# Kernel tuning notes

Measured on AMD Instinct MI355X. Metric: run time of the kernel, lower is better.

Reference implementation:

```python
import jax, jax.numpy as jnp
import numpy as np

N_NODES = 50000
N_EDGES = 800000
IN_DIM = 128
EMB = 128
EDGE_DIM = 16
N_LAYERS = 4
BATCH = 64


def setup_inputs() -> dict:
    key = jax.random.key(0)
    ks = jax.random.split(key, 12)
    x = jax.random.normal(ks[0], (N_NODES, IN_DIM), dtype=jnp.float32)
    edge_index = jax.random.randint(ks[1], (2, N_EDGES), 0, N_NODES, dtype=jnp.int64)
    edge_attr = jax.random.normal(ks[2], (N_EDGES, EDGE_DIM), dtype=jnp.float32)
    batch = jnp.sort(jax.random.randint(ks[3], (N_NODES,), 0, BATCH, dtype=jnp.int64))

    def glorot(k, shape):
        fan_in = shape[-2]
        return jax.random.normal(k, shape, dtype=jnp.float32) / jnp.sqrt(jnp.float32(fan_in))

    msg_in = 2 * EMB + EDGE_DIM  # [h_src, h_dst, edge_attr]
    upd_in = 2 * EMB             # [h, aggregated_messages]
    return {
        "x": x,
        "edge_index": edge_index,
        "edge_attr": edge_attr,
        "batch": batch,
        "W_in": glorot(ks[4], (IN_DIM, EMB)),
        "b_in": jnp.zeros((EMB,), jnp.float32),
        "W_msg": glorot(ks[5], (N_LAYERS, msg_in, EMB)),
        "b_msg": jnp.zeros((N_LAYERS, EMB), jnp.float32),
        "W_upd": glorot(ks[6], (N_LAYERS, upd_in, EMB)),
        "b_upd": jnp.zeros((N_LAYERS, EMB), jnp.float32),
        "W_pred": glorot(ks[7], (EMB, 1)),
        "b_pred": jnp.zeros((1,), jnp.float32),
    }


def reference(x, edge_index, edge_attr, batch,
              W_in, b_in, W_msg, b_msg, W_upd, b_upd, W_pred, b_pred):
    n_nodes = x.shape[0]
    src, dst = edge_index[0], edge_index[1]

    # lin_in
    h = x @ W_in + b_in  # [N, EMB]

    # stacked message-passing layers with residual adds
    for l in range(W_msg.shape[0]):  # small fixed layer loop
        # per-edge message: relu(Linear([h_src, h_dst, e]))
        m_in = jnp.concatenate([h[src], h[dst], edge_attr], axis=-1)  # [E, 2*EMB+ED]
        m = jax.nn.relu(m_in @ W_msg[l] + b_msg[l])                    # [E, EMB]
        # sum-aggregate messages at destination nodes
        agg = jax.ops.segment_sum(m, dst, num_segments=n_nodes)       # [N, EMB]
        # node update: relu(Linear([h, agg])); residual add (h = h + conv(h))
        u_in = jnp.concatenate([h, agg], axis=-1)                      # [N, 2*EMB]
        h = h + jax.nn.relu(u_in @ W_upd[l] + b_upd[l])

    # global mean pool over graphs in the batch
    counts = jax.ops.segment_sum(jnp.ones((n_nodes,), h.dtype), batch, num_segments=BATCH)
    h_graph = jax.ops.segment_sum(h, batch, num_segments=BATCH) / jnp.maximum(counts, 1.0)[:, None]

    # lin_pred + view(-1)
    out = h_graph @ W_pred + b_pred  # [BATCH, 1]
    return out.reshape(-1)
```

## Files before the change

### kernel.cpp

```cpp
#include <hip/hip_runtime.h>


#define THREADS 256

typedef __attribute__((ext_vector_type(8))) short short8v;
typedef __attribute__((ext_vector_type(4))) float f32x4;

__device__ inline unsigned short f2bf(float f)
{
    unsigned int u = __float_as_uint(f);
    return (unsigned short)((u + 0x7FFFu + ((u >> 16) & 1u)) >> 16);
}

__global__ __launch_bounds__(THREADS)
void wconv_all(const float* __restrict__ W_in, const float* __restrict__ W_msg,
               const float* __restrict__ W_upd, unsigned short* __restrict__ wbf)
{
    int b = blockIdx.x;
    int job, kb;
    if (b < 576) { job = b >> 6; kb = b & 63; }
    else         { int r = b - 576; job = 9 + (r >> 7); kb = r & 127; }

    const float* src;
    unsigned short* dst;
    int K;
    if (job == 0)      { src = W_in;                                  dst = wbf;                       K = 128; }
    else if (job <= 4) { int l = job - 1; src = W_msg + (size_t)l * 272 * 128;             dst = wbf + 16384  + l * 16384; K = 128; }
    else if (job <= 8) { int l = job - 5; src = W_msg + (size_t)l * 272 * 128 + 128 * 128; dst = wbf + 81920  + l * 16384; K = 128; }
    else               { int l = job - 9; src = W_upd + (size_t)l * 256 * 128;             dst = wbf + 147456 + l * 32768; K = 256; }

    int i = kb * 256 + threadIdx.x;
    int k = i >> 7, n = i & 127;
    dst[n * K + k] = f2bf(src[i]);
}

__global__ __launch_bounds__(THREADS)
void f32_to_bf16(const float* __restrict__ in, unsigned short* __restrict__ out, int n4)
{
    int i = blockIdx.x * blockDim.x + threadIdx.x;
    int stride = gridDim.x * blockDim.x;
    for (; i < n4; i += stride) {
        float4 v = reinterpret_cast<const float4*>(in)[i];
        unsigned int lo = f2bf(v.x) | ((unsigned int)f2bf(v.y) << 16);
        unsigned int hi = f2bf(v.z) | ((unsigned int)f2bf(v.w) << 16);
        reinterpret_cast<uint2*>(out)[i] = make_uint2(lo, hi);
    }
}

template<bool RELU, bool RESID, bool WF32>
__global__ __launch_bounds__(THREADS)
void gemm_bf16(const unsigned short* __restrict__ X1, const unsigned short* __restrict__ X2,
               const unsigned short* __restrict__ Wt, const float* __restrict__ bias,
               const float* __restrict__ resid, float* __restrict__ Cf,
               unsigned short* __restrict__ Cbf, int M, int K)
{
    __shared__ unsigned short Als[64 * 40];
    __shared__ unsigned short Bls[128 * 40];

    const int t = threadIdx.x;
    const int w = t >> 6;
    const int l = t & 63;
    const int r  = l & 15;
    const int kb = l >> 4;
    const int mBase = blockIdx.x * 64;

    f32x4 acc[8];
#pragma unroll
    for (int c = 0; c < 8; c++) acc[c] = (f32x4){0.f, 0.f, 0.f, 0.f};

    const int am = t >> 2;
    const int ak = (t & 3) * 8;
    const int agr = min(mBase + am, M - 1);

    const int c0 = t, c1 = t + 256;
    const int bn0 = c0 >> 2, bk0 = (c0 & 3) * 8;
    const int bn1 = c1 >> 2, bk1 = (c1 & 3) * 8;

    for (int k0 = 0; k0 < K; k0 += 32) {
        const unsigned short* Xs = X1;
        int ko = k0;
        if (k0 >= 128) { Xs = X2; ko = k0 - 128; }

        short8v xv  = *reinterpret_cast<const short8v*>(Xs + (size_t)agr * 128 + ko + ak);
        short8v wv0 = *reinterpret_cast<const short8v*>(Wt + (size_t)bn0 * K + k0 + bk0);
        short8v wv1 = *reinterpret_cast<const short8v*>(Wt + (size_t)bn1 * K + k0 + bk1);

        __syncthreads();

        *reinterpret_cast<short8v*>(&Als[am * 40 + ak])   = xv;
        *reinterpret_cast<short8v*>(&Bls[bn0 * 40 + bk0]) = wv0;
        *reinterpret_cast<short8v*>(&Bls[bn1 * 40 + bk1]) = wv1;

        __syncthreads();

        const short8v a = *reinterpret_cast<const short8v*>(&Als[(w * 16 + r) * 40 + kb * 8]);
#pragma unroll
        for (int c = 0; c < 8; c++) {
            const short8v b = *reinterpret_cast<const short8v*>(&Bls[(c * 16 + r) * 40 + kb * 8]);
            acc[c] = __builtin_amdgcn_mfma_f32_16x16x32_bf16(a, b, acc[c], 0, 0, 0);
        }
    }

    const int rbase = mBase + w * 16 + kb * 4;
#pragma unroll
    for (int c = 0; c < 8; c++) {
        const int gc = c * 16 + r;
        float bv = bias ? bias[gc] : 0.f;
#pragma unroll
        for (int j = 0; j < 4; j++) {
            int gr = rbase + j;
            if (gr >= M) continue;
            float v = acc[c][j] + bv;
            if (RELU)  v = fmaxf(v, 0.f);
            if (RESID) v += resid[(size_t)gr * 128 + gc];
            if (WF32)  Cf[(size_t)gr * 128 + gc] = v;
            Cbf[(size_t)gr * 128 + gc] = f2bf(v);
        }
    }
}

__global__ __launch_bounds__(THREADS)
void zero_i32(int* __restrict__ p, int n)
{
    int i = blockIdx.x * blockDim.x + threadIdx.x;
    int stride = gridDim.x * blockDim.x;
    for (; i < n; i += stride) p[i] = 0;
}


__global__ __launch_bounds__(THREADS)
void csr_hist(const int* __restrict__ edst, int* __restrict__ deg, int nE)
{
    int i = blockIdx.x * blockDim.x + threadIdx.x;
    int stride = gridDim.x * blockDim.x;
    for (; i < nE; i += stride) atomicAdd(&deg[edst[i]], 1);
}

__global__ __launch_bounds__(THREADS)
void scan_stage1(const int* __restrict__ deg, int* __restrict__ incl,
                 int* __restrict__ psum, int n)
{
    __shared__ int buf[THREADS];
    const int t = threadIdx.x;
    const int base = blockIdx.x * 1024 + t * 4;

    int v0 = (base + 0 < n) ? deg[base + 0] : 0;
    int v1 = (base + 1 < n) ? deg[base + 1] : 0;
    int v2 = (base + 2 < n) ? deg[base + 2] : 0;
    int v3 = (base + 3 < n) ? deg[base + 3] : 0;
    const int s = v0 + v1 + v2 + v3;

    buf[t] = s;
    __syncthreads();
#pragma unroll
    for (int off = 1; off < THREADS; off <<= 1) {
        int x = (t >= off) ? buf[t - off] : 0;
        __syncthreads();
        buf[t] += x;
        __syncthreads();
    }
    const int excl = buf[t] - s;

    if (base + 0 < n) incl[base + 0] = excl + v0;
    if (base + 1 < n) incl[base + 1] = excl + v0 + v1;
    if (base + 2 < n) incl[base + 2] = excl + v0 + v1 + v2;
    if (base + 3 < n) incl[base + 3] = excl + s;
    if (t == THREADS - 1) psum[blockIdx.x] = buf[THREADS - 1];
}

__global__ __launch_bounds__(THREADS)
void scan_stage2(int* __restrict__ psum, int nb)
{
    __shared__ int buf[THREADS];
    const int t = threadIdx.x;
    int v = (t < nb) ? psum[t] : 0;
    buf[t] = v;
    __syncthreads();
#pragma unroll
    for (int off = 1; off < THREADS; off <<= 1) {
        int x = (t >= off) ? buf[t - off] : 0;
        __syncthreads();
        buf[t] += x;
        __syncthreads();
    }
    if (t < nb) psum[t] = buf[t] - v;
}

__global__ __launch_bounds__(THREADS)
void scan_stage3(const int* __restrict__ incl, const int* __restrict__ deg,
                 const int* __restrict__ psum, int* __restrict__ rowptr,
                 int* __restrict__ wp, int n, int nE)
{
    int i = blockIdx.x * blockDim.x + threadIdx.x;
    int stride = gridDim.x * blockDim.x;
    for (; i < n; i += stride) {
        int ex = incl[i] - deg[i] + psum[i >> 10];
        rowptr[i] = ex;
        wp[i]     = ex;
    }
    if (blockIdx.x == 0 && threadIdx.x == 0) rowptr[n] = nE;
}

__global__ __launch_bounds__(THREADS)
void csr_scatter(const int* __restrict__ esrc, const int* __restrict__ edst,
                 const float* __restrict__ eattr, int* __restrict__ wp,
                 int* __restrict__ col, float* __restrict__ eattrp, int nE)
{
    int i = blockIdx.x * blockDim.x + threadIdx.x;
    int stride = gridDim.x * blockDim.x;
    for (; i < nE; i += stride) {
        int d = edst[i];
        int pos = atomicAdd(&wp[d], 1);
        col[pos] = esrc[i];
        const float4* src4 = reinterpret_cast<const float4*>(eattr + (size_t)i * 16);
        float4*       dst4 = reinterpret_cast<float4*>(eattrp + (size_t)pos * 16);
        dst4[0] = src4[0]; dst4[1] = src4[1]; dst4[2] = src4[2]; dst4[3] = src4[3];
    }
}

__global__ __launch_bounds__(THREADS)
void edge_agg(const unsigned short* __restrict__ A, const unsigned short* __restrict__ Bb,
              const float* __restrict__ eattrp, const int* __restrict__ col,
              const int* __restrict__ rowptr, const float* __restrict__ Wm3,
              unsigned short* __restrict__ agg, int nN)
{
    __shared__ float W3s[16 * 128];
    const int t = threadIdx.x;

    *reinterpret_cast<float4*>(&W3s[t * 4])        = *reinterpret_cast<const float4*>(Wm3 + t * 4);
    *reinterpret_cast<float4*>(&W3s[1024 + t * 4]) = *reinterpret_cast<const float4*>(Wm3 + 1024 + t * 4);
    __syncthreads();

    const int lane = t & 63;
    const int wid  = __builtin_amdgcn_readfirstlane(t >> 6);
    const int d    = blockIdx.x * 4 + wid;
    if (d >= nN) return;

    float2 w[16];
#pragma unroll
    for (int k = 0; k < 16; k++)
        w[k] = *reinterpret_cast<const float2*>(&W3s[k * 128 + lane * 2]);

    const unsigned int bu = *reinterpret_cast<const unsigned int*>(Bb + (size_t)d * 128 + lane * 2);
    const float b0 = __uint_as_float(bu << 16);
    const float b1 = __uint_as_float(bu & 0xFFFF0000u);
    float2 acc = make_float2(0.f, 0.f);

    const int beg = rowptr[d], end = rowptr[d + 1];
    for (int e = beg; e < end; e++) {
        const int s = col[e];
        const unsigned int au = *reinterpret_cast<const unsigned int*>(A + (size_t)s * 128 + lane * 2);
        float vx = __uint_as_float(au << 16) + b0;
        float vy = __uint_as_float(au & 0xFFFF0000u) + b1;
        const float4* ea4 = reinterpret_cast<const float4*>(eattrp + (size_t)e * 16);
        const float4 e0 = ea4[0], e1 = ea4[1], e2 = ea4[2], e3 = ea4[3];
        const float ek[16] = {e0.x, e0.y, e0.z, e0.w, e1.x, e1.y, e1.z, e1.w,
                              e2.x, e2.y, e2.z, e2.w, e3.x, e3.y, e3.z, e3.w};
#pragma unroll
        for (int k = 0; k < 16; k++) {
            vx = fmaf(ek[k], w[k].x, vx);
            vy = fmaf(ek[k], w[k].y, vy);
        }
        acc.x += fmaxf(vx, 0.f);
        acc.y += fmaxf(vy, 0.f);
    }
    unsigned int o = (unsigned int)f2bf(acc.x) | ((unsigned int)f2bf(acc.y) << 16);
    *reinterpret_cast<unsigned int*>(agg + (size_t)d * 128 + lane * 2) = o;
}


__global__ __launch_bounds__(THREADS)
void pool_partial(const float* __restrict__ h, const int* __restrict__ batch,
                  float* __restrict__ hgsum, int n)
{
    const int t    = threadIdx.x;
    const int c    = t & 127;
    const int half = t >> 7;
    const int beg  = blockIdx.x * 256;
    const int end  = min(beg + 256, n);
    if (beg >= n) return;

    int   cur = -1;
    float acc = 0.f;
    for (int r = beg + half; r < end; r += 2) {
        int g = batch[r];
        if (g != cur) {
            if (cur >= 0) atomicAdd(&hgsum[(size_t)cur * 128 + c], acc);
            cur = g; acc = 0.f;
        }
        acc += h[(size_t)r * 128 + c];
    }
    if (cur >= 0) atomicAdd(&hgsum[(size_t)cur * 128 + c], acc);
}

__global__ __launch_bounds__(THREADS)
void pool_final(const float* __restrict__ hgsum, const int* __restrict__ batch,
                const float* __restrict__ Wp, const float* __restrict__ bp,
                float* __restrict__ out, int n)
{
    __shared__ float red[128];
    const int g = blockIdx.x;
    const int t = threadIdx.x;
    if (t >= 128) return;

    int lo, hi;
    {
        int a = 0, b = n;
        while (a < b) { int m = (a + b) >> 1; if (batch[m] < g) a = m + 1; else b = m; }
        lo = a;
        b = n;
        while (a < b) { int m = (a + b) >> 1; if (batch[m] < g + 1) a = m + 1; else b = m; }
        hi = a;
    }
    const int cnt = hi - lo;

    float v = hgsum[(size_t)g * 128 + t] / (float)max(cnt, 1);
    red[t] = v * Wp[t];
    __syncthreads();
    for (int off = 64; off > 0; off >>= 1) {
        if (t < off) red[t] += red[t + off];
        __syncthreads();
    }
    if (t == 0) out[g] = red[0] + bp[0];
}

extern "C" void kernel_launch(void* const* d_in, const int* in_sizes, int n_in,
                              void* d_out, int out_size, void* d_ws, size_t ws_size,
                              hipStream_t stream)
{
    const float* x      = (const float*)d_in[0];
    const int*   ei     = (const int*)  d_in[1];
    const float* eattr  = (const float*)d_in[2];
    const int*   batch  = (const int*)  d_in[3];
    const float* W_in   = (const float*)d_in[4];
    const float* b_in   = (const float*)d_in[5];
    const float* W_msg  = (const float*)d_in[6];
    const float* b_msg  = (const float*)d_in[7];
    const float* W_upd  = (const float*)d_in[8];
    const float* b_upd  = (const float*)d_in[9];
    const float* W_pred = (const float*)d_in[10];
    const float* b_pred = (const float*)d_in[11];
    float* out = (float*)d_out;

    const int nN = in_sizes[0] / 128;
    const int nE = in_sizes[1] / 2;
    const int* esrc = ei;
    const int* edst = ei + nE;

    float* h      = (float*)d_ws;
    float* eattrp = h + (size_t)nN * 128;
    float* hgsum  = eattrp + (size_t)nE * 16;
    unsigned short* xbf    = (unsigned short*)(hgsum + 8192);
    unsigned short* h_bf   = xbf    + (size_t)nN * 128;
    unsigned short* A_bf   = h_bf   + (size_t)nN * 128;
    unsigned short* Bb_bf  = A_bf   + (size_t)nN * 128;
    unsigned short* agg_bf = Bb_bf  + (size_t)nN * 128;
    unsigned short* wbf    = agg_bf + (size_t)nN * 128;
    unsigned short* wt_in  = wbf;
    unsigned short* wt_m1  = wbf + 16384;
    unsigned short* wt_m2  = wbf + 81920;
    unsigned short* wt_up  = wbf + 147456;
    int*   rowptr = (int*)(wbf + 278528);
    int*   wp     = rowptr + (nN + 1);
    int*   deg    = wp     + nN;
    int*   incl   = deg    + nN;
    int*   psum   = incl   + nN;
    int*   col    = psum   + 256;

    dim3 blk(THREADS);
    const int gx = (nN + 63) / 64;
    const int nChunks = (nN + 1023) / 1024;

    wconv_all<<<1088, blk, 0, stream>>>(W_in, W_msg, W_upd, wbf);
    f32_to_bf16<<<1024, blk, 0, stream>>>(x, xbf, nN * 128 / 4);

    zero_i32<<<64, blk, 0, stream>>>(deg, nN);
    csr_hist<<<256, blk, 0, stream>>>(edst, deg, nE);
    scan_stage1<<<nChunks, blk, 0, stream>>>(deg, incl, psum, nN);
    scan_stage2<<<1, blk, 0, stream>>>(psum, nChunks);
    scan_stage3<<<64, blk, 0, stream>>>(incl, deg, psum, rowptr, wp, nN, nE);
    csr_scatter<<<256, blk, 0, stream>>>(esrc, edst, eattr, wp, col, eattrp, nE);

    gemm_bf16<false, false, true><<<gx, blk, 0, stream>>>(xbf, nullptr, wt_in, b_in, nullptr, h, h_bf, nN, 128);

    for (int l = 0; l < 4; l++) {
        const float* Wm3 = W_msg + (size_t)l * 272 * 128 + 256 * 128;
        const float* bm  = b_msg + l * 128;
        const float* bu  = b_upd + l * 128;

        gemm_bf16<false, false, false><<<gx, blk, 0, stream>>>(h_bf, nullptr, wt_m1 + l * 16384, nullptr, nullptr, nullptr, A_bf,  nN, 128);
        gemm_bf16<false, false, false><<<gx, blk, 0, stream>>>(h_bf, nullptr, wt_m2 + l * 16384, bm,      nullptr, nullptr, Bb_bf, nN, 128);

        edge_agg<<<(nN + 3) / 4, blk, 0, stream>>>(A_bf, Bb_bf, eattrp, col, rowptr, Wm3, agg_bf, nN);

        gemm_bf16<true, true, true><<<gx, blk, 0, stream>>>(h_bf, agg_bf, wt_up + l * 32768, bu, h, h, h_bf, nN, 256);
    }

    zero_i32<<<16, blk, 0, stream>>>((int*)hgsum, 64 * 128);
    pool_partial<<<(nN + 255) / 256, blk, 0, stream>>>(h, batch, hgsum, nN);
    pool_final<<<64, blk, 0, stream>>>(hgsum, batch, W_pred, b_pred, out, nN);
}
```

Baseline: 666.7 us.

## Load GEMM operands directly into registers and unroll edge aggregation by two

The bf16 GEMM drops its LDS staging and both __syncthreads. Each wave now loads its A rows and the weight fragments straight from global memory into MFMA operand registers. Each wave computes 32 rows with two accumulator sets, so the block tile grows to 128 rows, and K becomes a template parameter. The edge aggregation loop also processes two edges per iteration to expose more memory-level parallelism, at the cost of more register pressure and redundant weight reads from L1/L2 across waves.

```diff
diff --git a/kernel.cpp b/kernel.cpp
--- a/kernel.cpp
+++ b/kernel.cpp
@@ -47,74 +47,63 @@
     }
 }
 
-template<bool RELU, bool RESID, bool WF32>
-__global__ __launch_bounds__(THREADS)
-void gemm_bf16(const unsigned short* __restrict__ X1, const unsigned short* __restrict__ X2,
-               const unsigned short* __restrict__ Wt, const float* __restrict__ bias,
-               const float* __restrict__ resid, float* __restrict__ Cf,
-               unsigned short* __restrict__ Cbf, int M, int K)
-{
-    __shared__ unsigned short Als[64 * 40];
-    __shared__ unsigned short Bls[128 * 40];
-
+template<bool RELU, bool RESID, bool WF32, int K>
+__global__ __launch_bounds__(THREADS, 2)
+void gemm_direct(const unsigned short* __restrict__ X1, const unsigned short* __restrict__ X2,
+                 const unsigned short* __restrict__ Wt, const float* __restrict__ bias,
+                 const float* __restrict__ resid, float* __restrict__ Cf,
+                 unsigned short* __restrict__ Cbf, int M)
+{
     const int t = threadIdx.x;
     const int w = t >> 6;
     const int l = t & 63;
     const int r  = l & 15;
     const int kb = l >> 4;
-    const int mBase = blockIdx.x * 64;
-
-    f32x4 acc[8];
-#pragma unroll
-    for (int c = 0; c < 8; c++) acc[c] = (f32x4){0.f, 0.f, 0.f, 0.f};
-
-    const int am = t >> 2;
-    const int ak = (t & 3) * 8;
-    const int agr = min(mBase + am, M - 1);
-
-    const int c0 = t, c1 = t + 256;
-    const int bn0 = c0 >> 2, bk0 = (c0 & 3) * 8;
-    const int bn1 = c1 >> 2, bk1 = (c1 & 3) * 8;
+    const int mBase = blockIdx.x * 128 + w * 32;
+
+    f32x4 acc[2][8];
+#pragma unroll
+    for (int mi = 0; mi < 2; mi++)
+#pragma unroll
+        for (int c = 0; c < 8; c++) acc[mi][c] = (f32x4){0.f, 0.f, 0.f, 0.f};
+
+    const int row0 = min(mBase + r,      M - 1);
+    const int row1 = min(mBase + 16 + r, M - 1);
 
     for (int k0 = 0; k0 < K; k0 += 32) {
         const unsigned short* Xs = X1;
         int ko = k0;
-        if (k0 >= 128) { Xs = X2; ko = k0 - 128; }
-
-        short8v xv  = *reinterpret_cast<const short8v*>(Xs + (size_t)agr * 128 + ko + ak);
-        short8v wv0 = *reinterpret_cast<const short8v*>(Wt + (size_t)bn0 * K + k0 + bk0);
-        short8v wv1 = *reinterpret_cast<const short8v*>(Wt + (size_t)bn1 * K + k0 + bk1);
-
-        __syncthreads();
-
-        *reinterpret_cast<short8v*>(&Als[am * 40 + ak])   = xv;
-        *reinterpret_cast<short8v*>(&Bls[bn0 * 40 + bk0]) = wv0;
-        *reinterpret_cast<short8v*>(&Bls[bn1 * 40 + bk1]) = wv1;
-
-        __syncthreads();
-
-        const short8v a = *reinterpret_cast<const short8v*>(&Als[(w * 16 + r) * 40 + kb * 8]);
+        if (K == 256 && k0 >= 128) { Xs = X2; ko = k0 - 128; }
+        const int kk = ko + kb * 8;
+
+        const short8v a0 = *reinterpret_cast<const short8v*>(Xs + (size_t)row0 * 128 + kk);
+        const short8v a1 = *reinterpret_cast<const short8v*>(Xs + (size_t)row1 * 128 + kk);
+
 #pragma unroll
         for (int c = 0; c < 8; c++) {
-            const short8v b = *reinterpret_cast<const short8v*>(&Bls[(c * 16 + r) * 40 + kb * 8]);
-            acc[c] = __builtin_amdgcn_mfma_f32_16x16x32_bf16(a, b, acc[c], 0, 0, 0);
+            const short8v b = *reinterpret_cast<const short8v*>(Wt + (size_t)(c * 16 + r) * K + k0 + kb * 8);
+            acc[0][c] = __builtin_amdgcn_mfma_f32_16x16x32_bf16(a0, b, acc[0][c], 0, 0, 0);
+            acc[1][c] = __builtin_amdgcn_mfma_f32_16x16x32_bf16(a1, b, acc[1][c], 0, 0, 0);
         }
     }
 
-    const int rbase = mBase + w * 16 + kb * 4;
-#pragma unroll
-    for (int c = 0; c < 8; c++) {
-        const int gc = c * 16 + r;
-        float bv = bias ? bias[gc] : 0.f;
-#pragma unroll
-        for (int j = 0; j < 4; j++) {
-            int gr = rbase + j;
-            if (gr >= M) continue;
-            float v = acc[c][j] + bv;
-            if (RELU)  v = fmaxf(v, 0.f);
-            if (RESID) v += resid[(size_t)gr * 128 + gc];
-            if (WF32)  Cf[(size_t)gr * 128 + gc] = v;
-            Cbf[(size_t)gr * 128 + gc] = f2bf(v);
+#pragma unroll
+    for (int mi = 0; mi < 2; mi++) {
+        const int rbase = mBase + mi * 16 + kb * 4;
+#pragma unroll
+        for (int c = 0; c < 8; c++) {
+            const int gc = c * 16 + r;
+            float bv = bias ? bias[gc] : 0.f;
+#pragma unroll
+            for (int j = 0; j < 4; j++) {
+                int gr = rbase + j;
+                if (gr >= M) continue;
+                float v = acc[mi][c][j] + bv;
+                if (RELU)  v = fmaxf(v, 0.f);
+                if (RESID) v += resid[(size_t)gr * 128 + gc];
+                if (WF32)  Cf[(size_t)gr * 128 + gc] = v;
+                Cbf[(size_t)gr * 128 + gc] = f2bf(v);
+            }
         }
     }
 }
@@ -247,15 +236,45 @@
     float2 acc = make_float2(0.f, 0.f);
 
     const int beg = rowptr[d], end = rowptr[d + 1];
-    for (int e = beg; e < end; e++) {
+    int e = beg;
+    for (; e + 2 <= end; e += 2) {
+        const int s0 = col[e];
+        const int s1 = col[e + 1];
+        const unsigned int au0 = *reinterpret_cast<const unsigned int*>(A + (size_t)s0 * 128 + lane * 2);
+        const unsigned int au1 = *reinterpret_cast<const unsigned int*>(A + (size_t)s1 * 128 + lane * 2);
+        const float4* p0 = reinterpret_cast<const float4*>(eattrp + (size_t)e * 16);
+        const float4* p1 = reinterpret_cast<const float4*>(eattrp + (size_t)(e + 1) * 16);
+        const float4 e00 = p0[0], e01 = p0[1], e02 = p0[2], e03 = p0[3];
+        const float4 e10 = p1[0], e11 = p1[1], e12 = p1[2], e13 = p1[3];
+
+        float v0x = __uint_as_float(au0 << 16) + b0;
+        float v0y = __uint_as_float(au0 & 0xFFFF0000u) + b1;
+        float v1x = __uint_as_float(au1 << 16) + b0;
+        float v1y = __uint_as_float(au1 & 0xFFFF0000u) + b1;
+
+        const float ek0[16] = {e00.x, e00.y, e00.z, e00.w, e01.x, e01.y, e01.z, e01.w,
+                               e02.x, e02.y, e02.z, e02.w, e03.x, e03.y, e03.z, e03.w};
+        const float ek1[16] = {e10.x, e10.y, e10.z, e10.w, e11.x, e11.y, e11.z, e11.w,
+                               e12.x, e12.y, e12.z, e12.w, e13.x, e13.y, e13.z, e13.w};
+#pragma unroll
+        for (int k = 0; k < 16; k++) {
+            v0x = fmaf(ek0[k], w[k].x, v0x);
+            v0y = fmaf(ek0[k], w[k].y, v0y);
+            v1x = fmaf(ek1[k], w[k].x, v1x);
+            v1y = fmaf(ek1[k], w[k].y, v1y);
+        }
+        acc.x += fmaxf(v0x, 0.f) + fmaxf(v1x, 0.f);
+        acc.y += fmaxf(v0y, 0.f) + fmaxf(v1y, 0.f);
+    }
+    if (e < end) {
         const int s = col[e];
         const unsigned int au = *reinterpret_cast<const unsigned int*>(A + (size_t)s * 128 + lane * 2);
         float vx = __uint_as_float(au << 16) + b0;
         float vy = __uint_as_float(au & 0xFFFF0000u) + b1;
         const float4* ea4 = reinterpret_cast<const float4*>(eattrp + (size_t)e * 16);
-        const float4 e0 = ea4[0], e1 = ea4[1], e2 = ea4[2], e3 = ea4[3];
-        const float ek[16] = {e0.x, e0.y, e0.z, e0.w, e1.x, e1.y, e1.z, e1.w,
-                              e2.x, e2.y, e2.z, e2.w, e3.x, e3.y, e3.z, e3.w};
+        const float4 f0 = ea4[0], f1 = ea4[1], f2 = ea4[2], f3 = ea4[3];
+        const float ek[16] = {f0.x, f0.y, f0.z, f0.w, f1.x, f1.y, f1.z, f1.w,
+                              f2.x, f2.y, f2.z, f2.w, f3.x, f3.y, f3.z, f3.w};
 #pragma unroll
         for (int k = 0; k < 16; k++) {
             vx = fmaf(ek[k], w[k].x, vx);
@@ -368,7 +387,7 @@
     int*   col    = psum   + 256;
 
     dim3 blk(THREADS);
-    const int gx = (nN + 63) / 64;
+    const int gx2 = (nN + 127) / 128;
     const int nChunks = (nN + 1023) / 1024;
 
     wconv_all<<<1088, blk, 0, stream>>>(W_in, W_msg, W_upd, wbf);
@@ -381,19 +400,19 @@
     scan_stage3<<<64, blk, 0, stream>>>(incl, deg, psum, rowptr, wp, nN, nE);
     csr_scatter<<<256, blk, 0, stream>>>(esrc, edst, eattr, wp, col, eattrp, nE);
 
-    gemm_bf16<false, false, true><<<gx, blk, 0, stream>>>(xbf, nullptr, wt_in, b_in, nullptr, h, h_bf, nN, 128);
+    gemm_direct<false, false, true, 128><<<gx2, blk, 0, stream>>>(xbf, nullptr, wt_in, b_in, nullptr, h, h_bf, nN);
 
     for (int l = 0; l < 4; l++) {
         const float* Wm3 = W_msg + (size_t)l * 272 * 128 + 256 * 128;
         const float* bm  = b_msg + l * 128;
         const float* bu  = b_upd + l * 128;
 
-        gemm_bf16<false, false, false><<<gx, blk, 0, stream>>>(h_bf, nullptr, wt_m1 + l * 16384, nullptr, nullptr, nullptr, A_bf,  nN, 128);
-        gemm_bf16<false, false, false><<<gx, blk, 0, stream>>>(h_bf, nullptr, wt_m2 + l * 16384, bm,      nullptr, nullptr, Bb_bf, nN, 128);
+        gemm_direct<false, false, false, 128><<<gx2, blk, 0, stream>>>(h_bf, nullptr, wt_m1 + l * 16384, nullptr, nullptr, nullptr, A_bf,  nN);
+        gemm_direct<false, false, false, 128><<<gx2, blk, 0, stream>>>(h_bf, nullptr, wt_m2 + l * 16384, bm,      nullptr, nullptr, Bb_bf, nN);
 
         edge_agg<<<(nN + 3) / 4, blk, 0, stream>>>(A_bf, Bb_bf, eattrp, col, rowptr, Wm3, agg_bf, nN);
 
-        gemm_bf16<true, true, true><<<gx, blk, 0, stream>>>(h_bf, agg_bf, wt_up + l * 32768, bu, h, h, h_bf, nN, 256);
+        gemm_direct<true, true, true, 256><<<gx2, blk, 0, stream>>>(h_bf, agg_bf, wt_up + l * 32768, bu, h, h, h_bf, nN);
     }
 
     zero_i32<<<16, blk, 0, stream>>>((int*)hgsum, 64 * 128);
```

Result: slower. 780.6 us (+17.1%).
